# Optimization experiments

Hardware: AMD Instinct MI355X
Metric: run time of the kernel (lower is better)

## Reference

```python
import jax, jax.numpy as jnp
import numpy as np

T, B, H, L = 512, 128, 256, 2  # seq_len, batch, hidden(=input) size, num_layers


def setup_inputs() -> dict:
    key = jax.random.key(0)
    k0, k1, k2, k3, k4 = jax.random.split(key, 5)
    s = 1.0 / np.sqrt(H)  # PyTorch LSTM init range
    x = jax.random.normal(k0, (T, B, H), jnp.float32)
    W_ih = jax.random.uniform(k1, (L, 4 * H, H), jnp.float32, -s, s)
    W_hh = jax.random.uniform(k2, (L, 4 * H, H), jnp.float32, -s, s)
    b_ih = jax.random.uniform(k3, (L, 4 * H), jnp.float32, -s, s)
    b_hh = jax.random.uniform(k4, (L, 4 * H), jnp.float32, -s, s)
    return {"x": x, "W_ih": W_ih, "W_hh": W_hh, "b_ih": b_ih, "b_hh": b_hh}


def _lstm(x, W_ih, W_hh, b_ih, b_hh):
    Ln, fourH, _ = W_ih.shape
    Hh = fourH // 4
    Bn = x.shape[1]
    h0 = jnp.zeros((Ln, Bn, Hh), x.dtype)
    c0 = jnp.zeros((Ln, Bn, Hh), x.dtype)

    def step(carry, x_t):
        h, c = carry
        inp = x_t
        hs, cs = [], []
        for l in range(Ln):  # small static layer loop
            gates = inp @ W_ih[l].T + b_ih[l] + h[l] @ W_hh[l].T + b_hh[l]
            gi, gf, gg, go = jnp.split(gates, 4, axis=-1)
            gi = jax.nn.sigmoid(gi)
            gf = jax.nn.sigmoid(gf)
            gg = jnp.tanh(gg)
            go = jax.nn.sigmoid(go)
            c_new = gf * c[l] + gi * gg
            h_new = go * jnp.tanh(c_new)
            hs.append(h_new)
            cs.append(c_new)
            inp = h_new
        return (jnp.stack(hs), jnp.stack(cs)), inp

    (hT, cT), out = jax.lax.scan(step, (h0, c0), x)
    return out, hT, cT


def reference(x, W_ih, W_hh, b_ih, b_hh):
    # Returns (output [T,B,H], h_n [L,B,H], c_n [L,B,H]) as in DPLSTM.forward
    return _lstm(x, W_ih, W_hh, b_ih, b_hh)
```

## Files before the change

### kernel.cpp

```cpp
#include <hip/hip_runtime.h>
#include <math.h>

#define T_LEN 512
#define BATCH 128
#define HID   256
#define BH    (BATCH*HID)

__device__ __forceinline__ float frcp(float d) {
    float r = __builtin_amdgcn_rcpf(d);
    return r * fmaf(-d, r, 2.0f);
}
__device__ __forceinline__ float sigmoid_f(float v) {
    return frcp(1.f + __expf(-v));
}
__device__ __forceinline__ float tanh_f(float v) {
    v = fminf(fmaxf(v, -15.f), 15.f);
    const float e = __expf(2.f * v);
    return (e - 1.f) * frcp(e + 1.f);
}
__device__ __forceinline__ float4 ldf4(const float* p) {
    return *reinterpret_cast<const float4*>(p);
}
__device__ __forceinline__ void fma4(float4& a, const float4 v, const float4 w) {
    a.x = fmaf(v.x, w.x, a.x);
    a.y = fmaf(v.y, w.y, a.y);
    a.z = fmaf(v.z, w.z, a.z);
    a.w = fmaf(v.w, w.w, a.w);
}
__device__ __forceinline__ float hsum4(const float4 a) {
    return (a.x + a.y) + (a.z + a.w);
}
__device__ __forceinline__ void pin4(float4& v) {
    asm volatile("" : "+v"(v.x), "+v"(v.y), "+v"(v.z), "+v"(v.w));
}
__device__ __forceinline__ void astore(float* p, float v) {
    __hip_atomic_store(p, v, __ATOMIC_RELAXED, __HIP_MEMORY_SCOPE_AGENT);
}
__device__ __forceinline__ float2 af2(const float* p) {
    unsigned long long u = __hip_atomic_load((const unsigned long long*)p,
                                             __ATOMIC_RELAXED, __HIP_MEMORY_SCOPE_AGENT);
    union { unsigned long long u; float2 f; } c; c.u = u;
    return c.f;
}
__device__ __forceinline__ float4 af4(const float* p) {
    const float2 a = af2(p), b = af2(p + 2);
    return make_float4(a.x, a.y, b.x, b.y);
}
template<int CTRL>
__device__ __forceinline__ float dpp_mv(float x) {
    return __int_as_float(__builtin_amdgcn_update_dpp(
        0, __float_as_int(x), CTRL, 0xF, 0xF, true));
}
__device__ __forceinline__ float red16(float x) {
    x += dpp_mv<0x111>(x);
    x += dpp_mv<0x112>(x);
    x += dpp_mv<0x114>(x);
    x += dpp_mv<0x118>(x);
    return x;
}

__global__ __launch_bounds__(256)
__attribute__((amdgpu_waves_per_eu(2, 2)))
void lstm_persist(
    const float* __restrict__ x,
    const float* __restrict__ Wih, const float* __restrict__ Whh,
    const float* __restrict__ bih, const float* __restrict__ bhh,
    float* __restrict__ out,
    float* __restrict__ h0buf,
    float* __restrict__ h1buf,
    int* __restrict__ flags)
{
    __shared__ float ls_in[8 * 640];
    __shared__ float ls_a [128 * 4];
    __shared__ float ls_ax[128 * 4];
    __shared__ float ls_c [128];

    const int tid = threadIdx.x;
    const int bid = blockIdx.x;
    const int bg = bid & 15;
    const int layer = (bid >> 4) & 1;
    const int jt = bid >> 5;
    const int jp = tid >> 4;
    const int kc = tid & 15;
    const int j = jt * 16 + jp;
    const int Bg0 = bg * 8;

    const float* Wih_l = Wih + (size_t)layer * 4 * HID * HID;
    const float* Whh_l = Whh + (size_t)layer * 4 * HID * HID;
    const float* bih_l = bih + layer * 4 * HID;
    const float* bhh_l = bhh + layer * 4 * HID;

    float4 wih[4][4], whh[4][4];
    float bias[4];
    #pragma unroll
    for (int g = 0; g < 4; ++g) {
        const int row = g * HID + j;
        const float* pih = Wih_l + (size_t)row * HID + kc * 16;
        const float* phh = Whh_l + (size_t)row * HID + kc * 16;
        #pragma unroll
        for (int m = 0; m < 4; ++m) {
            wih[g][m] = ldf4(pih + m * 4);
            pin4(wih[g][m]);
            whh[g][m] = ldf4(phh + m * 4);
            pin4(whh[g][m]);
        }
        bias[g] = bih_l[row] + bhh_l[row];
        asm volatile("" : "+v"(bias[g]));
    }

    if (tid < 128) {
        ls_c[tid] = 0.f;
        #pragma unroll
        for (int g = 0; g < 4; ++g) ls_ax[tid * 4 + g] = 0.f;
    }

    int* myflag = flags + bg * 32 + layer * 16 + jt;

    #pragma unroll 1
    for (int s = 0; s <= T_LEN + 2; ++s) {
        if (s > 0 && tid < 32) {
            const int thr = (layer == 0 && tid >= 16) ? (s - 1) : s;
            const int* f = flags + bg * 32 + tid;
            while (__hip_atomic_load(f, __ATOMIC_RELAXED, __HIP_MEMORY_SCOPE_AGENT) < thr)
                __builtin_amdgcn_s_sleep(1);
        }
        __syncthreads();

        const bool crit = (layer == 0) ? (s >= 1 && s <= T_LEN) : (s >= 3);
        const bool xact = (layer == 0) ? (s < T_LEN) : (s >= 2 && s <= T_LEN + 1);
        const bool zeroh = (layer == 0) ? (s == 1) : (s == 3);

        if (crit || xact) {
            const float* ph0 = h0buf + (size_t)((s + 1) % 3) * BH;
            const float* ph1 = h1buf + (size_t)((s + 2) % 3) * BH;
            #pragma unroll
            for (int i = 0; i < 4; ++i) {
                const int F = tid + 256 * i;
                const int b = F >> 7;
                const int rr = F & 127;
                const size_t row = (size_t)(Bg0 + b) * HID + (rr & 63) * 4;
                float4 v = make_float4(0.f, 0.f, 0.f, 0.f);
                if ((rr >> 6) == 0) {
                    if (xact)
                        v = (layer == 0) ? ldf4(x + (size_t)s * BH + row)
                                         : af4(ph0 + row);
                } else if (crit && !zeroh) {
                    v = (layer == 0) ? af4(ph0 + row) : af4(ph1 + row);
                }
                *(float4*)(ls_in + b * 640 + (rr >> 2) * 20 + (rr & 3) * 4) = v;
            }
        }
        __syncthreads();

        if (crit) {
            #pragma unroll 2
            for (int b = 0; b < 8; ++b) {
                const float4* Lp = (const float4*)(ls_in + b * 640 + (16 + kc) * 20);
                const float4 i0 = Lp[0], i1 = Lp[1], i2 = Lp[2], i3 = Lp[3];
                float4 ac[4];
                #pragma unroll
                for (int g = 0; g < 4; ++g) ac[g] = make_float4(0.f, 0.f, 0.f, 0.f);
                #pragma unroll
                for (int g = 0; g < 4; ++g) {
                    fma4(ac[g], i0, whh[g][0]);
                    fma4(ac[g], i1, whh[g][1]);
                    fma4(ac[g], i2, whh[g][2]);
                    fma4(ac[g], i3, whh[g][3]);
                }
                const float a0 = red16(hsum4(ac[0]));
                const float a1 = red16(hsum4(ac[1]));
                const float a2 = red16(hsum4(ac[2]));
                const float a3 = red16(hsum4(ac[3]));
                if (kc == 15) {
                    const int cell = b * 16 + jp;
                    const float* axp = ls_ax + cell * 4;
                    float* ap = ls_a + cell * 4;
                    ap[0] = a0 + bias[0] + axp[0];
                    ap[1] = a1 + bias[1] + axp[1];
                    ap[2] = a2 + bias[2] + axp[2];
                    ap[3] = a3 + bias[3] + axp[3];
                }
            }
        }
        __syncthreads();

        if (crit && tid < 128) {
            const int bb = tid >> 4;
            const int jpp = tid & 15;
            const int t = (layer == 0) ? (s - 1) : (s - 3);
            float* hst = (layer == 0) ? (h0buf + (size_t)((s + 2) % 3) * BH)
                                      : (h1buf + (size_t)(s % 3) * BH);
            const bool last = (t == T_LEN - 1);
            const float* ap = ls_a + tid * 4;
            const float gi = sigmoid_f(ap[0]);
            const float gf = sigmoid_f(ap[1]);
            const float gg = tanh_f   (ap[2]);
            const float go = sigmoid_f(ap[3]);
            const float cold = ls_c[tid];
            const float cnew = fmaf(gf, cold, gi * gg);
            ls_c[tid] = cnew;
            const float h = go * tanh_f(cnew);
            const int B = Bg0 + bb;
            const int jg = jt * 16 + jpp;
            astore(hst + (size_t)B * HID + jg, h);
            if (layer == 1)
                out[(size_t)t * BH + (size_t)B * HID + jg] = h;
            if (last) {
                float* hn  = out + (size_t)T_LEN * BH;
                float* cnp = hn + 2 * BH;
                hn [(size_t)layer * BH + (size_t)B * HID + jg] = h;
                cnp[(size_t)layer * BH + (size_t)B * HID + jg] = cnew;
            }
        }
        __syncthreads();
        if (s <= T_LEN + 1 && tid == 0)
            __hip_atomic_store(myflag, s + 1, __ATOMIC_RELAXED, __HIP_MEMORY_SCOPE_AGENT);

        if (xact) {
            #pragma unroll 2
            for (int b = 0; b < 8; ++b) {
                const float4* Lp = (const float4*)(ls_in + b * 640 + kc * 20);
                const float4 i0 = Lp[0], i1 = Lp[1], i2 = Lp[2], i3 = Lp[3];
                float4 ac[4];
                #pragma unroll
                for (int g = 0; g < 4; ++g) ac[g] = make_float4(0.f, 0.f, 0.f, 0.f);
                #pragma unroll
                for (int g = 0; g < 4; ++g) {
                    fma4(ac[g], i0, wih[g][0]);
                    fma4(ac[g], i1, wih[g][1]);
                    fma4(ac[g], i2, wih[g][2]);
                    fma4(ac[g], i3, wih[g][3]);
                }
                const float a0 = red16(hsum4(ac[0]));
                const float a1 = red16(hsum4(ac[1]));
                const float a2 = red16(hsum4(ac[2]));
                const float a3 = red16(hsum4(ac[3]));
                if (kc == 15) {
                    float* axp = ls_ax + (b * 16 + jp) * 4;
                    axp[0] = a0;
                    axp[1] = a1;
                    axp[2] = a2;
                    axp[3] = a3;
                }
            }
        }
    }
}

extern "C" void kernel_launch(void* const* d_in, const int* in_sizes, int n_in,
                              void* d_out, int out_size, void* d_ws, size_t ws_size,
                              hipStream_t stream) {
    const float* x   = (const float*)d_in[0];
    const float* Wih = (const float*)d_in[1];
    const float* Whh = (const float*)d_in[2];
    const float* bih = (const float*)d_in[3];
    const float* bhh = (const float*)d_in[4];
    float* out = (float*)d_out;

    float* h0 = (float*)d_ws;
    float* h1 = h0 + 3 * BH;
    int* flags = (int*)(h1 + 3 * BH);

    hipLaunchKernelGGL(lstm_persist, dim3(512), dim3(256), 0, stream,
                       x, Wih, Whh, bih, bhh, out, h0, h1, flags);
}
```

Baseline: 3.591 ms.

## Split recurrent and input projections across two thread halves with double-buffered ax

The block grows to 512 threads. The first 256 threads hold W_hh and compute the recurrent gate sums, while the second 256 hold W_ih and compute the input projection for the next step concurrently, instead of running it serially after the flag store. The input-projection buffer is double-buffered by step parity so both halves can run in the same phase. Each thread now holds half as many weight registers, and waves per EU rise to 4. The recurrent path's critical loop no longer waits behind the input GEMV, at the cost of more threads per block and x-projection work now sitting before the barrier ahead of the cell update.

```diff
diff --git a/kernel.cpp b/kernel.cpp
--- a/kernel.cpp
+++ b/kernel.cpp
@@ -59,8 +59,8 @@
     return x;
 }
 
-__global__ __launch_bounds__(256)
-__attribute__((amdgpu_waves_per_eu(2, 2)))
+__global__ __launch_bounds__(512)
+__attribute__((amdgpu_waves_per_eu(4, 4)))
 void lstm_persist(
     const float* __restrict__ x,
     const float* __restrict__ Wih, const float* __restrict__ Whh,
@@ -72,7 +72,7 @@
 {
     __shared__ float ls_in[8 * 640];
     __shared__ float ls_a [128 * 4];
-    __shared__ float ls_ax[128 * 4];
+    __shared__ float ls_ax[2][128 * 4];
     __shared__ float ls_c [128];
 
     const int tid = threadIdx.x;
@@ -80,39 +80,37 @@
     const int bg = bid & 15;
     const int layer = (bid >> 4) & 1;
     const int jt = bid >> 5;
-    const int jp = tid >> 4;
-    const int kc = tid & 15;
+    const int tl = tid & 255;
+    const int jp = tl >> 4;
+    const int kc = tl & 15;
     const int j = jt * 16 + jp;
     const int Bg0 = bg * 8;
+    const bool iscrit = (tid < 256);
 
     const float* Wih_l = Wih + (size_t)layer * 4 * HID * HID;
     const float* Whh_l = Whh + (size_t)layer * 4 * HID * HID;
     const float* bih_l = bih + layer * 4 * HID;
     const float* bhh_l = bhh + layer * 4 * HID;
 
-    float4 wih[4][4], whh[4][4];
+    const float* Wsel = iscrit ? Whh_l : Wih_l;
+    float4 w[4][4];
     float bias[4];
     #pragma unroll
     for (int g = 0; g < 4; ++g) {
         const int row = g * HID + j;
-        const float* pih = Wih_l + (size_t)row * HID + kc * 16;
-        const float* phh = Whh_l + (size_t)row * HID + kc * 16;
+        const float* pw = Wsel + (size_t)row * HID + kc * 16;
         #pragma unroll
         for (int m = 0; m < 4; ++m) {
-            wih[g][m] = ldf4(pih + m * 4);
-            pin4(wih[g][m]);
-            whh[g][m] = ldf4(phh + m * 4);
-            pin4(whh[g][m]);
+            w[g][m] = ldf4(pw + m * 4);
+            pin4(w[g][m]);
         }
         bias[g] = bih_l[row] + bhh_l[row];
         asm volatile("" : "+v"(bias[g]));
     }
 
-    if (tid < 128) {
-        ls_c[tid] = 0.f;
-        #pragma unroll
-        for (int g = 0; g < 4; ++g) ls_ax[tid * 4 + g] = 0.f;
-    }
+    if (tid < 128) ls_c[tid] = 0.f;
+
+    const int lrow = iscrit ? (16 + kc) : kc;
 
     int* myflag = flags + bg * 32 + layer * 16 + jt;
 
@@ -134,8 +132,8 @@
             const float* ph0 = h0buf + (size_t)((s + 1) % 3) * BH;
             const float* ph1 = h1buf + (size_t)((s + 2) % 3) * BH;
             #pragma unroll
-            for (int i = 0; i < 4; ++i) {
-                const int F = tid + 256 * i;
+            for (int i = 0; i < 2; ++i) {
+                const int F = tid + 512 * i;
                 const int b = F >> 7;
                 const int rr = F & 127;
                 const size_t row = (size_t)(Bg0 + b) * HID + (rr & 63) * 4;
@@ -152,20 +150,20 @@
         }
         __syncthreads();
 
-        if (crit) {
+        if (iscrit ? crit : xact) {
             #pragma unroll 2
             for (int b = 0; b < 8; ++b) {
-                const float4* Lp = (const float4*)(ls_in + b * 640 + (16 + kc) * 20);
+                const float4* Lp = (const float4*)(ls_in + b * 640 + lrow * 20);
                 const float4 i0 = Lp[0], i1 = Lp[1], i2 = Lp[2], i3 = Lp[3];
                 float4 ac[4];
                 #pragma unroll
                 for (int g = 0; g < 4; ++g) ac[g] = make_float4(0.f, 0.f, 0.f, 0.f);
                 #pragma unroll
                 for (int g = 0; g < 4; ++g) {
-                    fma4(ac[g], i0, whh[g][0]);
-                    fma4(ac[g], i1, whh[g][1]);
-                    fma4(ac[g], i2, whh[g][2]);
-                    fma4(ac[g], i3, whh[g][3]);
+                    fma4(ac[g], i0, w[g][0]);
+                    fma4(ac[g], i1, w[g][1]);
+                    fma4(ac[g], i2, w[g][2]);
+                    fma4(ac[g], i3, w[g][3]);
                 }
                 const float a0 = red16(hsum4(ac[0]));
                 const float a1 = red16(hsum4(ac[1]));
@@ -173,12 +171,20 @@
                 const float a3 = red16(hsum4(ac[3]));
                 if (kc == 15) {
                     const int cell = b * 16 + jp;
-                    const float* axp = ls_ax + cell * 4;
-                    float* ap = ls_a + cell * 4;
-                    ap[0] = a0 + bias[0] + axp[0];
-                    ap[1] = a1 + bias[1] + axp[1];
-                    ap[2] = a2 + bias[2] + axp[2];
-                    ap[3] = a3 + bias[3] + axp[3];
+                    if (iscrit) {
+                        const float* axp = &ls_ax[s & 1][cell * 4];
+                        float* ap = ls_a + cell * 4;
+                        ap[0] = a0 + bias[0] + axp[0];
+                        ap[1] = a1 + bias[1] + axp[1];
+                        ap[2] = a2 + bias[2] + axp[2];
+                        ap[3] = a3 + bias[3] + axp[3];
+                    } else {
+                        float* axp = &ls_ax[(s + 1) & 1][cell * 4];
+                        axp[0] = a0;
+                        axp[1] = a1;
+                        axp[2] = a2;
+                        axp[3] = a3;
+                    }
                 }
             }
         }
@@ -215,35 +221,6 @@
         __syncthreads();
         if (s <= T_LEN + 1 && tid == 0)
             __hip_atomic_store(myflag, s + 1, __ATOMIC_RELAXED, __HIP_MEMORY_SCOPE_AGENT);
-
-        if (xact) {
-            #pragma unroll 2
-            for (int b = 0; b < 8; ++b) {
-                const float4* Lp = (const float4*)(ls_in + b * 640 + kc * 20);
-                const float4 i0 = Lp[0], i1 = Lp[1], i2 = Lp[2], i3 = Lp[3];
-                float4 ac[4];
-                #pragma unroll
-                for (int g = 0; g < 4; ++g) ac[g] = make_float4(0.f, 0.f, 0.f, 0.f);
-                #pragma unroll
-                for (int g = 0; g < 4; ++g) {
-                    fma4(ac[g], i0, wih[g][0]);
-                    fma4(ac[g], i1, wih[g][1]);
-                    fma4(ac[g], i2, wih[g][2]);
-                    fma4(ac[g], i3, wih[g][3]);
-                }
-                const float a0 = red16(hsum4(ac[0]));
-                const float a1 = red16(hsum4(ac[1]));
-                const float a2 = red16(hsum4(ac[2]));
-                const float a3 = red16(hsum4(ac[3]));
-                if (kc == 15) {
-                    float* axp = ls_ax + (b * 16 + jp) * 4;
-                    axp[0] = a0;
-                    axp[1] = a1;
-                    axp[2] = a2;
-                    axp[3] = a3;
-                }
-            }
-        }
     }
 }
 
@@ -261,6 +238,6 @@
     float* h1 = h0 + 3 * BH;
     int* flags = (int*)(h1 + 3 * BH);
 
-    hipLaunchKernelGGL(lstm_persist, dim3(512), dim3(256), 0, stream,
+    hipLaunchKernelGGL(lstm_persist, dim3(512), dim3(512), 0, stream,
                        x, Wih, Whh, bih, bhh, out, h0, h1, flags);
 }
```

Result: slower. 4.268 ms (+18.9%).
